# Optimization experiments

Measured on AMD Instinct MI355X. Metric: run time of the kernel, lower is better.

The kernel has to match this reference:

```python
import jax, jax.numpy as jnp
import numpy as np

N = 100000      # nodes
E = 3200000     # edges (avg degree 32)
NFEAT = 512
NHID = 256
NCLASS = 40
NLAYERS = 8
T1 = 5
T2 = 5
G1 = 1
G2 = 1
BETA = 0.5      # weight_beta
LAMDA = 0.5
ALPHA = 0.1
EPS = 1e-5


def ortho_trans(weight, T, groups):
    """Newton-Schulz orthogonalization (Ortho_Trans.forward)."""
    g = groups
    Z = weight.reshape(g, weight.shape[0] // g, -1)          # [g, d, k]
    Zc = Z - Z.mean(axis=-1, keepdims=True)
    S = jnp.einsum('gik,gjk->gij', Zc, Zc)                   # covariance [g, d, d]
    eye = jnp.eye(S.shape[-1], dtype=S.dtype)
    S = S + EPS * eye
    norm_S = jnp.sqrt(jnp.sum(S * S, axis=(1, 2), keepdims=True))  # fro norm
    S = S / norm_S
    B0 = jnp.broadcast_to(eye, S.shape)

    def body(B, _):
        B3 = B @ B @ B                                       # matrix_power3
        return 1.5 * B - 0.5 * (B3 @ S), None                # baddbmm(1.5,B,-0.5,B3,S)

    Bt, _ = jax.lax.scan(body, B0, None, length=T)
    W = (Bt @ Zc) / jnp.sqrt(norm_S)
    return W.reshape(weight.shape)


def setup_inputs() -> dict:
    key = jax.random.key(0)
    ks = jax.random.split(key, 8)
    stdv = 1.0 / np.sqrt(NHID)
    return {
        'x': jax.random.normal(ks[0], (N, NFEAT), dtype=jnp.float32),
        'edge_src': jax.random.randint(ks[1], (E,), 0, N, dtype=jnp.int32),
        'edge_dst': jax.random.randint(ks[2], (E,), 0, N, dtype=jnp.int32),
        'edge_weight': jax.random.uniform(ks[3], (E,), dtype=jnp.float32),
        'W0': jax.random.normal(ks[4], (NHID, NFEAT), dtype=jnp.float32) * 0.05,
        'b0': jnp.zeros((NHID,), dtype=jnp.float32),
        'convW': jax.random.uniform(ks[5], (NLAYERS, NHID, NHID), dtype=jnp.float32,
                                    minval=-stdv, maxval=stdv),
        'W1': jax.random.normal(ks[6], (NCLASS, NHID), dtype=jnp.float32) * 0.05,
        'b1': jnp.zeros((NCLASS,), dtype=jnp.float32),
    }


def reference(x, edge_src, edge_dst, edge_weight, W0, b0, convW, W1, b1):
    # fcs[0].weight is orthogonalized at init (Ortho=True)
    W0o = ortho_trans(W0, T1, G1)
    h = jax.nn.relu(x @ W0o.T + b0)                          # [N, NHID]
    h0 = h
    I = jnp.eye(NHID, dtype=h.dtype)
    ls = jnp.arange(1, NLAYERS + 1, dtype=h.dtype)

    def layer(h, inp):
        W, l = inp
        theta = jnp.log(LAMDA / l + 1.0)
        # sparse spmm: hi = adj @ h
        msgs = edge_weight[:, None] * h[edge_src]            # [E, NHID]
        hi = jax.ops.segment_sum(msgs, edge_dst, num_segments=N)
        support = (1.0 - ALPHA) * hi + ALPHA * h0            # variant=False -> r == support
        we = BETA * W + (1.0 - BETA) * I
        t = ortho_trans(we, T2, G2)
        out = jax.nn.relu(theta * (support @ t) + (1.0 - theta) * support)
        return out, None

    h, _ = jax.lax.scan(layer, h, (convW, ls))
    logits = h @ W1.T + b1
    return jax.nn.log_softmax(logits, axis=1)
```

## Files before the change

### kernel.cpp

```cpp
#include <hip/hip_runtime.h>
#include <math.h>

#define NNODES 100000
#define NEDGE  3200000
#define NF     512
#define NH     256
#define NC     40
#define NLAY   8
#define EPSV   1e-5f

typedef __attribute__((ext_vector_type(8))) short short8;
typedef __attribute__((ext_vector_type(4))) float floatx4;



__device__ __forceinline__ float block_sum_256(float v) {
    __shared__ float sb[8];
    #pragma unroll
    for (int off = 32; off; off >>= 1) v += __shfl_down(v, off, 64);
    if ((threadIdx.x & 63) == 0) sb[threadIdx.x >> 6] = v;
    __syncthreads();
    return sb[0] + sb[1] + sb[2] + sb[3];
}

__device__ __forceinline__ unsigned short bf16_rte(float a) {
    unsigned int u = __float_as_uint(a);
    return (unsigned short)((u + 0x7fffu + ((u >> 16) & 1u)) >> 16);
}
__device__ __forceinline__ unsigned int pack_bf2(float a, float b) {
    unsigned int ua = __float_as_uint(a), ub = __float_as_uint(b);
    ua = (ua + 0x7fffu + ((ua >> 16) & 1u)) >> 16;
    ub = (ub + 0x7fffu + ((ub >> 16) & 1u)) & 0xffff0000u;
    return ua | ub;
}


__global__ void k_hist(const int* __restrict__ dst, int* __restrict__ counts, int n) {
    int i = blockIdx.x * 256 + threadIdx.x;
    if (i < n) atomicAdd(&counts[dst[i]], 1);
}

__global__ void k_scan1(const int* __restrict__ in, int* __restrict__ out,
                        int* __restrict__ bsum, int n) {
    __shared__ int s[1024];
    int t = threadIdx.x, g = blockIdx.x * 1024 + t;
    int v = (g < n) ? in[g] : 0;
    s[t] = v; __syncthreads();
    for (int off = 1; off < 1024; off <<= 1) {
        int u = (t >= off) ? s[t - off] : 0;
        __syncthreads();
        s[t] += u;
        __syncthreads();
    }
    if (g < n) out[g] = s[t] - v;
    if (t == 1023) bsum[blockIdx.x] = s[1023];
}

__global__ void k_scan2(int* __restrict__ bsum, int nb) {
    __shared__ int s[128];
    int t = threadIdx.x;
    int v = (t < nb) ? bsum[t] : 0;
    s[t] = v; __syncthreads();
    for (int off = 1; off < 128; off <<= 1) {
        int u = (t >= off) ? s[t - off] : 0;
        __syncthreads();
        s[t] += u;
        __syncthreads();
    }
    if (t < nb) bsum[t] = s[t] - v;
}

__global__ void k_scan3(int* __restrict__ out, const int* __restrict__ bsum, int n) {
    int g = blockIdx.x * 1024 + threadIdx.x;
    if (g < n) out[g] += bsum[blockIdx.x];
}

__global__ void k_scatter(const int* __restrict__ src, const int* __restrict__ dst,
                          const float* __restrict__ w, const int* __restrict__ rstart,
                          int* __restrict__ cursor, unsigned int* __restrict__ epack, int n) {
    int i = blockIdx.x * 256 + threadIdx.x;
    if (i < n) {
        int d = dst[i];
        int pos = rstart[d] + atomicAdd(&cursor[d], 1);
        unsigned int wb = bf16_rte(w[i]) & 0x7FFFu;
        epack[pos] = ((unsigned int)src[i] << 15) | wb;
    }
}


__global__ void k_xbf16(const float* __restrict__ X, unsigned short* __restrict__ Xb, long n8) {
    long i = (long)blockIdx.x * 256 + threadIdx.x;
    if (i >= n8) return;
    const float* p = X + i * 8;
    float4 a = *(const float4*)p;
    float4 b = *(const float4*)(p + 4);
    uint4 o;
    o.x = pack_bf2(a.x, a.y); o.y = pack_bf2(a.z, a.w);
    o.z = pack_bf2(b.x, b.y); o.w = pack_bf2(b.z, b.w);
    *(uint4*)(Xb + i * 8) = o;
}


__global__ void k_zc0(const float* __restrict__ W0, float* __restrict__ Zc0) {
    int r = blockIdx.x, t = threadIdx.x;
    float a = W0[r * NF + t];
    float b = W0[r * NF + 256 + t];
    float mean = block_sum_256(a + b) * (1.0f / 512.0f);
    Zc0[r * NF + t]       = a - mean;
    Zc0[r * NF + 256 + t] = b - mean;
}

__global__ void k_zcC(const float* __restrict__ convW, float* __restrict__ ZcC) {
    int g = blockIdx.x >> 8, r = blockIdx.x & 255, t = threadIdx.x;
    float v = 0.5f * convW[((size_t)g * NH + r) * NH + t] + ((r == t) ? 0.5f : 0.0f);
    float mean = block_sum_256(v) * (1.0f / 256.0f);
    ZcC[((size_t)g * NH + r) * NH + t] = v - mean;
}

__global__ __launch_bounds__(256) void k_gram(const float* __restrict__ Zc0,
                                              const float* __restrict__ ZcC,
                                              float* __restrict__ S) {
    const int b = blockIdx.z;
    const float* A = (b == 0) ? Zc0 : (ZcC + (size_t)(b - 1) * 65536);
    const int K = (b == 0) ? 512 : 256;
    const int r0 = blockIdx.y * 64, c0 = blockIdx.x * 64;
    __shared__ float As[32][76], Bs[32][76];
    const int t = threadIdx.x, tx = t & 15, ty = t >> 4;
    const int lr = t >> 2, lk = (t & 3) * 4;
    float acc[4][4] = {};
    for (int k0 = 0; k0 < K; k0 += 32) {
        float4 a0 = *(const float4*)(A + (size_t)(r0 + lr) * K + k0 + lk);
        float4 a1 = *(const float4*)(A + (size_t)(r0 + lr) * K + k0 + lk + 16);
        As[lk + 0][lr] = a0.x; As[lk + 1][lr] = a0.y; As[lk + 2][lr] = a0.z; As[lk + 3][lr] = a0.w;
        As[lk + 16][lr] = a1.x; As[lk + 17][lr] = a1.y; As[lk + 18][lr] = a1.z; As[lk + 19][lr] = a1.w;
        float4 b0 = *(const float4*)(A + (size_t)(c0 + lr) * K + k0 + lk);
        float4 b1 = *(const float4*)(A + (size_t)(c0 + lr) * K + k0 + lk + 16);
        Bs[lk + 0][lr] = b0.x; Bs[lk + 1][lr] = b0.y; Bs[lk + 2][lr] = b0.z; Bs[lk + 3][lr] = b0.w;
        Bs[lk + 16][lr] = b1.x; Bs[lk + 17][lr] = b1.y; Bs[lk + 18][lr] = b1.z; Bs[lk + 19][lr] = b1.w;
        __syncthreads();
        #pragma unroll
        for (int kk = 0; kk < 32; kk++) {
            float a[4], bb[4];
            *(float4*)&a[0]  = *(const float4*)&As[kk][ty * 4];
            *(float4*)&bb[0] = *(const float4*)&Bs[kk][tx * 4];
            #pragma unroll
            for (int i = 0; i < 4; i++)
                #pragma unroll
                for (int j = 0; j < 4; j++) acc[i][j] = fmaf(a[i], bb[j], acc[i][j]);
        }
        __syncthreads();
    }
    #pragma unroll
    for (int i = 0; i < 4; i++)
        #pragma unroll
        for (int j = 0; j < 4; j++) {
            int r = r0 + ty * 4 + i, c = c0 + tx * 4 + j;
            float v = acc[i][j];
            if (r == c) v += EPSV;
            S[(size_t)b * 65536 + r * NH + c] = v;
        }
}

__global__ void k_fro(const float* __restrict__ S, float* __restrict__ scales) {
    __shared__ float sb[8];
    const int b = blockIdx.x, t = threadIdx.x;
    const float* p = S + (size_t)b * 65536;
    float s = 0.f;
    for (int i = t; i < 65536; i += 256) { float v = p[i]; s = fmaf(v, v, s); }
    #pragma unroll
    for (int off = 32; off; off >>= 1) s += __shfl_down(s, off, 64);
    if ((t & 63) == 0) sb[t >> 6] = s;
    __syncthreads();
    if (t == 0) {
        float nrm = sqrtf(sb[0] + sb[1] + sb[2] + sb[3]);
        scales[b]      = 1.0f / nrm;
        scales[16 + b] = rsqrtf(nrm);
    }
}

__global__ void k_initB1(const float* __restrict__ S, const float* __restrict__ scales,
                         float* __restrict__ B) {
    int i = blockIdx.x * 256 + threadIdx.x;
    int b = i >> 16, m = i & 65535;
    float v = -0.5f * scales[b] * S[i];
    if ((m >> 8) == (m & 255)) v += 1.5f;
    B[i] = v;
}

__global__ __launch_bounds__(256) void k_ns_pair(const float* __restrict__ Bb,
                                                 const float* __restrict__ Smat,
                                                 float* __restrict__ T1b,
                                                 float* __restrict__ T2b) {
    const int b = blockIdx.z;
    const int bb = (b < 9) ? b : b - 9;
    const float* A  = Bb + (size_t)bb * 65536;
    const float* Bm = (b < 9) ? A : (Smat + (size_t)bb * 65536);
    float* C = (b < 9) ? (T1b + (size_t)bb * 65536) : (T2b + (size_t)bb * 65536);
    const int r0 = blockIdx.y * 64, c0 = blockIdx.x * 64;
    __shared__ float As[32][76], Bs[32][76];
    const int t = threadIdx.x, tx = t & 15, ty = t >> 4;
    const int lr = t >> 2, lk = (t & 3) * 4;
    const int bk = t >> 3, bc = (t & 7) * 8;
    float acc[4][4] = {};
    for (int k0 = 0; k0 < 256; k0 += 32) {
        float4 a0 = *(const float4*)(A + (size_t)(r0 + lr) * 256 + k0 + lk);
        float4 a1 = *(const float4*)(A + (size_t)(r0 + lr) * 256 + k0 + lk + 16);
        As[lk + 0][lr] = a0.x; As[lk + 1][lr] = a0.y; As[lk + 2][lr] = a0.z; As[lk + 3][lr] = a0.w;
        As[lk + 16][lr] = a1.x; As[lk + 17][lr] = a1.y; As[lk + 18][lr] = a1.z; As[lk + 19][lr] = a1.w;
        float4 b0 = *(const float4*)(Bm + (size_t)(k0 + bk) * 256 + c0 + bc);
        float4 b1 = *(const float4*)(Bm + (size_t)(k0 + bk) * 256 + c0 + bc + 4);
        *(float4*)&Bs[bk][bc]     = b0;
        *(float4*)&Bs[bk][bc + 4] = b1;
        __syncthreads();
        #pragma unroll
        for (int kk = 0; kk < 32; kk++) {
            float a[4], bb2[4];
            *(float4*)&a[0]   = *(const float4*)&As[kk][ty * 4];
            *(float4*)&bb2[0] = *(const float4*)&Bs[kk][tx * 4];
            #pragma unroll
            for (int i = 0; i < 4; i++)
                #pragma unroll
                for (int j = 0; j < 4; j++) acc[i][j] = fmaf(a[i], bb2[j], acc[i][j]);
        }
        __syncthreads();
    }
    #pragma unroll
    for (int i = 0; i < 4; i++)
        #pragma unroll
        for (int j = 0; j < 4; j++)
            C[(size_t)(r0 + ty * 4 + i) * 256 + c0 + tx * 4 + j] = acc[i][j];
}

__global__ __launch_bounds__(256) void k_small_nn(const float* __restrict__ A0,
                                                  const float* __restrict__ B0,
                                                  float* __restrict__ C0,
                                                  int sA, int sB, int sC,
                                                  int K, int Ncols, int mode,
                                                  const float* __restrict__ scale) {
    const int b = blockIdx.z;
    const float* A = A0 + (size_t)b * sA;
    const float* Bm = B0 + (size_t)b * sB;
    float* C = C0 + (size_t)b * sC;
    const int r0 = blockIdx.y * 64, c0 = blockIdx.x * 64;
    __shared__ float As[32][76], Bs[32][76];
    const int t = threadIdx.x, tx = t & 15, ty = t >> 4;
    const int lr = t >> 2, lk = (t & 3) * 4;
    const int bk = t >> 3, bc = (t & 7) * 8;
    float acc[4][4] = {};
    for (int k0 = 0; k0 < K; k0 += 32) {
        float4 a0 = *(const float4*)(A + (size_t)(r0 + lr) * K + k0 + lk);
        float4 a1 = *(const float4*)(A + (size_t)(r0 + lr) * K + k0 + lk + 16);
        As[lk + 0][lr] = a0.x; As[lk + 1][lr] = a0.y; As[lk + 2][lr] = a0.z; As[lk + 3][lr] = a0.w;
        As[lk + 16][lr] = a1.x; As[lk + 17][lr] = a1.y; As[lk + 18][lr] = a1.z; As[lk + 19][lr] = a1.w;
        float4 b0 = *(const float4*)(Bm + (size_t)(k0 + bk) * Ncols + c0 + bc);
        float4 b1 = *(const float4*)(Bm + (size_t)(k0 + bk) * Ncols + c0 + bc + 4);
        *(float4*)&Bs[bk][bc]     = b0;
        *(float4*)&Bs[bk][bc + 4] = b1;
        __syncthreads();
        #pragma unroll
        for (int kk = 0; kk < 32; kk++) {
            float a[4], bb[4];
            *(float4*)&a[0]  = *(const float4*)&As[kk][ty * 4];
            *(float4*)&bb[0] = *(const float4*)&Bs[kk][tx * 4];
            #pragma unroll
            for (int i = 0; i < 4; i++)
                #pragma unroll
                for (int j = 0; j < 4; j++) acc[i][j] = fmaf(a[i], bb[j], acc[i][j]);
        }
        __syncthreads();
    }
    #pragma unroll
    for (int i = 0; i < 4; i++)
        #pragma unroll
        for (int j = 0; j < 4; j++) {
            size_t idx = (size_t)(r0 + ty * 4 + i) * Ncols + c0 + tx * 4 + j;
            if (mode == 1) C[idx] = 1.5f * C[idx] - 0.5f * scale[b] * acc[i][j];
            else C[idx] = scale[b] * acc[i][j];
        }
}


__global__ void k_prepM(const float* __restrict__ tbuf, unsigned short* __restrict__ Mpack) {
    int idx = blockIdx.x * 256 + threadIdx.x;
    int lane = idx & 63;
    int tg   = (idx >> 6) & 15;
    int s    = (idx >> 10) & 1;
    int c    = (idx >> 11) & 3;
    int l    = idx >> 13;
    float theta = logf(0.5f / (float)(l + 1) + 1.0f);
    float mtheta = 1.0f - theta;
    int n  = tg * 16 + (lane & 15);
    int k0 = c * 64 + s * 32 + (lane >> 4) * 8;
    const float* T = tbuf + (size_t)l * 65536;
    unsigned short o[8];
    #pragma unroll
    for (int j = 0; j < 8; j++) {
        int kp = k0 + j;
        int kn = (kp & 0xC0) | ((kp & 3) << 4) | ((kp >> 2) & 15);
        float v = theta * T[(size_t)kn * 256 + n] + ((kn == n) ? mtheta : 0.0f);
        o[j] = bf16_rte(v);
    }
    *(uint4*)(Mpack + (size_t)idx * 8) = *(uint4*)o;
}

__global__ void k_prepW0(const float* __restrict__ W0o, unsigned short* __restrict__ Wpack) {
    int idx = blockIdx.x * 256 + threadIdx.x;
    int lane = idx & 63;
    int tg   = (idx >> 6) & 15;
    int s    = (idx >> 10) & 1;
    int c    = idx >> 11;
    int n  = tg * 16 + (lane & 15);
    int k0 = c * 64 + s * 32 + (lane >> 4) * 8;
    const float* p = W0o + (size_t)n * NF + k0;
    unsigned short o[8];
    #pragma unroll
    for (int j = 0; j < 8; j++) o[j] = bf16_rte(p[j]);
    *(uint4*)(Wpack + (size_t)idx * 8) = *(uint4*)o;
}


__global__ __launch_bounds__(256) void k_fc0_mfma(const unsigned short* __restrict__ Xb,
                                                  const unsigned short* __restrict__ Wp,
                                                  const float* __restrict__ bias,
                                                  unsigned char* __restrict__ h0u8,
                                                  float* __restrict__ h0scale) {
    __shared__ int rmax[64];
    const int t = threadIdx.x, lane = t & 63, w = t >> 6;
    const int q = lane >> 4, m = lane & 15;
    const int r0 = blockIdx.x * 64;
    if (t < 64) rmax[t] = 0;
    floatx4 acc[4][4] = {};
    #pragma unroll
    for (int c = 0; c < 8; c++) {
        #pragma unroll
        for (int s = 0; s < 2; s++) {
            short8 afr[4];
            #pragma unroll
            for (int i = 0; i < 4; i++) {
                int row = r0 + i * 16 + m; if (row > NNODES - 1) row = NNODES - 1;
                afr[i] = *(const short8*)(Xb + (size_t)row * NF + c * 64 + s * 32 + q * 8);
            }
            #pragma unroll
            for (int tg = 0; tg < 4; tg++) {
                short8 bfr = *(const short8*)(Wp + (size_t)c * 16384 + s * 8192
                                              + (w * 4 + tg) * 512 + lane * 8);
                #pragma unroll
                for (int i = 0; i < 4; i++)
                    acc[i][tg] = __builtin_amdgcn_mfma_f32_16x16x32_bf16(afr[i], bfr, acc[i][tg], 0, 0, 0);
            }
        }
    }
    #pragma unroll
    for (int tg = 0; tg < 4; tg++) {
        float bv = bias[w * 64 + tg * 16 + m];
        #pragma unroll
        for (int i = 0; i < 4; i++)
            #pragma unroll
            for (int r = 0; r < 4; r++)
                acc[i][tg][r] = fmaxf(acc[i][tg][r] + bv, 0.f);
    }
    __syncthreads();
    #pragma unroll
    for (int i = 0; i < 4; i++)
        #pragma unroll
        for (int r = 0; r < 4; r++) {
            float mx = fmaxf(fmaxf(acc[i][0][r], acc[i][1][r]),
                             fmaxf(acc[i][2][r], acc[i][3][r]));
            mx = fmaxf(mx, __shfl_xor(mx, 1));
            mx = fmaxf(mx, __shfl_xor(mx, 2));
            mx = fmaxf(mx, __shfl_xor(mx, 4));
            mx = fmaxf(mx, __shfl_xor(mx, 8));
            if (m == 0) atomicMax(&rmax[i * 16 + q * 4 + r], __float_as_int(mx));
        }
    __syncthreads();
    #pragma unroll
    for (int i = 0; i < 4; i++)
        #pragma unroll
        for (int r = 0; r < 4; r++) {
            int row = r0 + i * 16 + q * 4 + r;
            if (row >= NNODES) continue;
            float rm = __int_as_float(rmax[i * 16 + q * 4 + r]);
            float qs = rm > 0.f ? 255.0f / rm : 0.f;
            unsigned int b0 = (unsigned int)fmaf(acc[i][0][r], qs, 0.5f);
            unsigned int b1 = (unsigned int)fmaf(acc[i][1][r], qs, 0.5f);
            unsigned int b2 = (unsigned int)fmaf(acc[i][2][r], qs, 0.5f);
            unsigned int b3 = (unsigned int)fmaf(acc[i][3][r], qs, 0.5f);
            *(unsigned int*)(h0u8 + (size_t)row * NH + w * 64 + m * 4) =
                b0 | (b1 << 8) | (b2 << 16) | (b3 << 24);
        }
    if (t < 64 && r0 + t < NNODES)
        h0scale[r0 + t] = __int_as_float(rmax[t]) * (1.0f / 255.0f);
}


__global__ __launch_bounds__(256) void k_spmm(const int* __restrict__ rstart,
                                              const int* __restrict__ counts,
                                              const unsigned int* __restrict__ epack,
                                              const unsigned char* __restrict__ hu8,
                                              const float* __restrict__ hscale,
                                              const unsigned char* __restrict__ h0u8,
                                              const float* __restrict__ h0scale,
                                              unsigned short* __restrict__ supbf) {
    __shared__ int2 se[4][64];
    const int wv = threadIdx.x >> 6, lane = threadIdx.x & 63;
    const int node = blockIdx.x * 4 + wv;
    const int start = rstart[node], deg = counts[node];
    float a0 = 0.f, a1 = 0.f, a2 = 0.f, a3 = 0.f;
    for (int base = 0; base < deg; base += 64) {
        int j = base + lane;
        if (j < deg) {
            unsigned int u = epack[start + j];
            int s = (int)(u >> 15);
            float wt = __uint_as_float((u & 0x7FFFu) << 16);
            se[wv][lane] = make_int2(s, __float_as_int(wt * hscale[s] * 0.9f));
        }
        int mm = deg - base; if (mm > 64) mm = 64;
        int e = 0;
        for (; e + 8 <= mm; e += 8) {
            float ww[8]; unsigned int g[8];
            #pragma unroll
            for (int u = 0; u < 8; u++) {
                int2 ed = se[wv][e + u];
                ww[u] = __int_as_float(ed.y);
                g[u] = *(const unsigned int*)(hu8 + ((size_t)ed.x << 8) + (lane << 2));
            }
            #pragma unroll
            for (int u = 0; u < 8; u++) {
                a0 = fmaf(ww[u], (float)(g[u] & 0xFFu), a0);
                a1 = fmaf(ww[u], (float)((g[u] >> 8) & 0xFFu), a1);
                a2 = fmaf(ww[u], (float)((g[u] >> 16) & 0xFFu), a2);
                a3 = fmaf(ww[u], (float)(g[u] >> 24), a3);
            }
        }
        for (; e < mm; e++) {
            int2 ed = se[wv][e];
            float ww = __int_as_float(ed.y);
            unsigned int g = *(const unsigned int*)(hu8 + ((size_t)ed.x << 8) + (lane << 2));
            a0 = fmaf(ww, (float)(g & 0xFFu), a0);
            a1 = fmaf(ww, (float)((g >> 8) & 0xFFu), a1);
            a2 = fmaf(ww, (float)((g >> 16) & 0xFFu), a2);
            a3 = fmaf(ww, (float)(g >> 24), a3);
        }
    }
    unsigned int rg = *(const unsigned int*)(h0u8 + ((size_t)node << 8) + (lane << 2));
    float rs = h0scale[node] * 0.1f;
    float o0 = fmaf(rs, (float)(rg & 0xFFu), a0);
    float o1 = fmaf(rs, (float)((rg >> 8) & 0xFFu), a1);
    float o2 = fmaf(rs, (float)((rg >> 16) & 0xFFu), a2);
    float o3 = fmaf(rs, (float)(rg >> 24), a3);
    uint2 ov;
    ov.x = pack_bf2(o0, o1);
    ov.y = pack_bf2(o2, o3);
    *(uint2*)(supbf + ((size_t)node << 8) + (lane << 2)) = ov;
}


__global__ __launch_bounds__(256) void k_gemm_layer(const unsigned short* __restrict__ Sbf,
                                                    const unsigned short* __restrict__ Mp,
                                                    unsigned char* __restrict__ out_u8,
                                                    float* __restrict__ out_scale,
                                                    unsigned short* __restrict__ out_bf) {
    __shared__ int rmax[64];
    const int t = threadIdx.x, lane = t & 63, w = t >> 6;
    const int q = lane >> 4, m = lane & 15;
    const int r0 = blockIdx.x * 64;
    if (t < 64) rmax[t] = 0;
    floatx4 acc[4][4] = {};
    #pragma unroll
    for (int c = 0; c < 4; c++) {
        #pragma unroll
        for (int s = 0; s < 2; s++) {
            short8 afr[4];
            #pragma unroll
            for (int i = 0; i < 4; i++) {
                int row = r0 + i * 16 + m; if (row > NNODES - 1) row = NNODES - 1;
                afr[i] = *(const short8*)(Sbf + (size_t)row * NH + c * 64 + s * 32 + q * 8);
            }
            #pragma unroll
            for (int tg = 0; tg < 4; tg++) {
                short8 bfr = *(const short8*)(Mp + (size_t)c * 16384 + s * 8192
                                              + (w * 4 + tg) * 512 + lane * 8);
                #pragma unroll
                for (int i = 0; i < 4; i++)
                    acc[i][tg] = __builtin_amdgcn_mfma_f32_16x16x32_bf16(afr[i], bfr, acc[i][tg], 0, 0, 0);
            }
        }
    }
    #pragma unroll
    for (int i = 0; i < 4; i++)
        #pragma unroll
        for (int tg = 0; tg < 4; tg++)
            #pragma unroll
            for (int r = 0; r < 4; r++)
                acc[i][tg][r] = fmaxf(acc[i][tg][r], 0.f);

    if (out_bf) {
        #pragma unroll
        for (int i = 0; i < 4; i++)
            #pragma unroll
            for (int tg = 0; tg < 4; tg++) {
                int col = w * 64 + tg * 16 + m;
                #pragma unroll
                for (int r = 0; r < 4; r++) {
                    int row = r0 + i * 16 + q * 4 + r;
                    if (row >= NNODES) continue;
                    out_bf[(size_t)row * NH + col] = bf16_rte(acc[i][tg][r]);
                }
            }
        return;
    }
    __syncthreads();
    #pragma unroll
    for (int i = 0; i < 4; i++)
        #pragma unroll
        for (int r = 0; r < 4; r++) {
            float mx = fmaxf(fmaxf(acc[i][0][r], acc[i][1][r]),
                             fmaxf(acc[i][2][r], acc[i][3][r]));
            mx = fmaxf(mx, __shfl_xor(mx, 1));
            mx = fmaxf(mx, __shfl_xor(mx, 2));
            mx = fmaxf(mx, __shfl_xor(mx, 4));
            mx = fmaxf(mx, __shfl_xor(mx, 8));
            if (m == 0) atomicMax(&rmax[i * 16 + q * 4 + r], __float_as_int(mx));
        }
    __syncthreads();
    #pragma unroll
    for (int i = 0; i < 4; i++)
        #pragma unroll
        for (int r = 0; r < 4; r++) {
            int row = r0 + i * 16 + q * 4 + r;
            if (row >= NNODES) continue;
            float rm = __int_as_float(rmax[i * 16 + q * 4 + r]);
            float qs = rm > 0.f ? 255.0f / rm : 0.f;
            unsigned int b0 = (unsigned int)fmaf(acc[i][0][r], qs, 0.5f);
            unsigned int b1 = (unsigned int)fmaf(acc[i][1][r], qs, 0.5f);
            unsigned int b2 = (unsigned int)fmaf(acc[i][2][r], qs, 0.5f);
            unsigned int b3 = (unsigned int)fmaf(acc[i][3][r], qs, 0.5f);
            *(unsigned int*)(out_u8 + (size_t)row * NH + w * 64 + m * 4) =
                b0 | (b1 << 8) | (b2 << 16) | (b3 << 24);
        }
    if (t < 64 && r0 + t < NNODES)
        out_scale[r0 + t] = __int_as_float(rmax[t]) * (1.0f / 255.0f);
}


__global__ __launch_bounds__(256) void k_logits(const unsigned short* __restrict__ hb,
                                                const float* __restrict__ W1,
                                                const float* __restrict__ b1,
                                                float* __restrict__ out, int nrows) {
    __shared__ float hs[32][260];
    __shared__ float Ws[40][260];
    __shared__ float ls[32][44];
    __shared__ float lse[32];
    const int t = threadIdx.x;
    const int row0 = blockIdx.x * 32;
    for (int i = t; i < 40 * 64; i += 256) {
        int c = i >> 6, k4 = i & 63;
        *(float4*)&Ws[c][k4 * 4] = *(const float4*)(W1 + (size_t)c * NH + k4 * 4);
    }
    for (int i = t; i < 32 * 32; i += 256) {
        int r = i >> 5, k8 = i & 31;
        int gr = row0 + r;
        uint4 v = make_uint4(0u, 0u, 0u, 0u);
        if (gr < nrows) v = *(const uint4*)(hb + ((size_t)gr << 8) + k8 * 8);
        float* d = &hs[r][k8 * 8];
        d[0] = __uint_as_float(v.x << 16); d[1] = __uint_as_float(v.x & 0xffff0000u);
        d[2] = __uint_as_float(v.y << 16); d[3] = __uint_as_float(v.y & 0xffff0000u);
        d[4] = __uint_as_float(v.z << 16); d[5] = __uint_as_float(v.z & 0xffff0000u);
        d[6] = __uint_as_float(v.w << 16); d[7] = __uint_as_float(v.w & 0xffff0000u);
    }
    __syncthreads();
    const int r = t & 31, cg = t >> 5;
    float acc[5];
    #pragma unroll
    for (int j = 0; j < 5; j++) acc[j] = b1[cg * 5 + j];
    for (int k = 0; k < NH; k++) {
        float hv = hs[r][k];
        #pragma unroll
        for (int j = 0; j < 5; j++) acc[j] = fmaf(hv, Ws[cg * 5 + j][k], acc[j]);
    }
    #pragma unroll
    for (int j = 0; j < 5; j++) ls[r][cg * 5 + j] = acc[j];
    __syncthreads();
    if (t < 32) {
        float m = -3.4e38f;
        for (int c = 0; c < NC; c++) m = fmaxf(m, ls[t][c]);
        float s = 0.f;
        for (int c = 0; c < NC; c++) s += expf(ls[t][c] - m);
        lse[t] = m + logf(s);
    }
    __syncthreads();
    for (int i = t; i < 32 * NC; i += 256) {
        int r2 = i / NC, c = i % NC;
        int gr = row0 + r2;
        if (gr < nrows) out[(size_t)gr * NC + c] = ls[r2][c] - lse[r2];
    }
}


extern "C" void kernel_launch(void* const* d_in, const int* in_sizes, int n_in,
                              void* d_out, int out_size, void* d_ws, size_t ws_size,
                              hipStream_t stream) {
    const float* x      = (const float*)d_in[0];
    const int*   e_src  = (const int*)d_in[1];
    const int*   e_dst  = (const int*)d_in[2];
    const float* e_w    = (const float*)d_in[3];
    const float* W0     = (const float*)d_in[4];
    const float* b0     = (const float*)d_in[5];
    const float* convW  = (const float*)d_in[6];
    const float* W1     = (const float*)d_in[7];
    const float* b1     = (const float*)d_in[8];
    float* out = (float*)d_out;

    char* ws = (char*)d_ws;
    const size_t OFF_H0U8   = 0;
    const size_t OFF_HU8A   = OFF_H0U8 + (size_t)NNODES * NH;
    const size_t OFF_HU8B   = OFF_HU8A + (size_t)NNODES * NH;
    const size_t OFF_H0SC   = OFF_HU8B + (size_t)NNODES * NH;
    const size_t OFF_SCA    = OFF_H0SC + (size_t)NNODES * 4;
    const size_t OFF_SCB    = OFF_SCA + (size_t)NNODES * 4;
    const size_t OFF_SUPBF  = OFF_SCB + (size_t)NNODES * 4;
    const size_t OFF_HBF    = OFF_SUPBF + (size_t)NNODES * NH * 2;
    const size_t OFF_XBF    = OFF_HBF + (size_t)NNODES * NH * 2;
    const size_t OFF_EPACK  = OFF_XBF + (size_t)NNODES * NF * 2;
    const size_t OFF_RSTART = OFF_EPACK + (size_t)NEDGE * 4;
    const size_t OFF_COUNTS = OFF_RSTART + (size_t)NNODES * 4;
    const size_t OFF_CURSOR = OFF_COUNTS + (size_t)NNODES * 4;
    const size_t OFF_BSUM   = OFF_CURSOR + (size_t)NNODES * 4;
    const size_t OFF_ZC0    = OFF_BSUM + 1024;
    const size_t OFF_ZCC    = OFF_ZC0 + 256 * 512 * 4;
    const size_t OFF_S      = OFF_ZCC + 8 * 65536 * 4;
    const size_t OFF_B      = OFF_S + 9 * 65536 * 4;
    const size_t OFF_T1     = OFF_B + 9 * 65536 * 4;
    const size_t OFF_T2     = OFF_T1 + 9 * 65536 * 4;
    const size_t OFF_T      = OFF_T2 + 9 * 65536 * 4;
    const size_t OFF_W0O    = OFF_T + 8 * 65536 * 4;
    const size_t OFF_SCALES = OFF_W0O + 256 * 512 * 4;
    const size_t OFF_MPACK  = OFF_SCALES + 1024;
    const size_t OFF_WPACK  = OFF_MPACK + 8 * 65536 * 2;

    unsigned char* h0u8 = (unsigned char*)(ws + OFF_H0U8);
    unsigned char* hu8A = (unsigned char*)(ws + OFF_HU8A);
    unsigned char* hu8B = (unsigned char*)(ws + OFF_HU8B);
    float* h0sc = (float*)(ws + OFF_H0SC);
    float* scA  = (float*)(ws + OFF_SCA);
    float* scB  = (float*)(ws + OFF_SCB);
    unsigned short* supbf = (unsigned short*)(ws + OFF_SUPBF);
    unsigned short* hbf   = (unsigned short*)(ws + OFF_HBF);
    unsigned short* xbf   = (unsigned short*)(ws + OFF_XBF);
    unsigned int* epack  = (unsigned int*)(ws + OFF_EPACK);
    int*    rstart = (int*)(ws + OFF_RSTART);
    int*    counts = (int*)(ws + OFF_COUNTS);
    int*    cursor = (int*)(ws + OFF_CURSOR);
    int*    bsum   = (int*)(ws + OFF_BSUM);
    float*  Zc0    = (float*)(ws + OFF_ZC0);
    float*  ZcC    = (float*)(ws + OFF_ZCC);
    float*  Smat   = (float*)(ws + OFF_S);
    float*  Bb     = (float*)(ws + OFF_B);
    float*  T1b    = (float*)(ws + OFF_T1);
    float*  T2b    = (float*)(ws + OFF_T2);
    float*  tbuf   = (float*)(ws + OFF_T);
    float*  W0o    = (float*)(ws + OFF_W0O);
    float*  scales = (float*)(ws + OFF_SCALES);
    unsigned short* Mpack = (unsigned short*)(ws + OFF_MPACK);
    unsigned short* Wpack = (unsigned short*)(ws + OFF_WPACK);

    (void)in_sizes; (void)n_in; (void)out_size; (void)ws_size;

    hipMemsetAsync(counts, 0, (size_t)NNODES * 4, stream);
    hipMemsetAsync(cursor, 0, (size_t)NNODES * 4, stream);
    k_hist<<<(NEDGE + 255) / 256, 256, 0, stream>>>(e_dst, counts, NEDGE);
    const int NB = (NNODES + 1023) / 1024;
    k_scan1<<<NB, 1024, 0, stream>>>(counts, rstart, bsum, NNODES);
    k_scan2<<<1, 128, 0, stream>>>(bsum, NB);
    k_scan3<<<NB, 1024, 0, stream>>>(rstart, bsum, NNODES);
    k_scatter<<<(NEDGE + 255) / 256, 256, 0, stream>>>(e_src, e_dst, e_w, rstart, cursor,
                                                       epack, NEDGE);

    const long N8 = (long)NNODES * NF / 8;
    k_xbf16<<<(int)((N8 + 255) / 256), 256, 0, stream>>>(x, xbf, N8);

    k_zc0<<<256, 256, 0, stream>>>(W0, Zc0);
    k_zcC<<<8 * 256, 256, 0, stream>>>(convW, ZcC);
    k_gram<<<dim3(4, 4, 9), 256, 0, stream>>>(Zc0, ZcC, Smat);
    k_fro<<<9, 256, 0, stream>>>(Smat, scales);
    k_initB1<<<9 * 256, 256, 0, stream>>>(Smat, scales, Bb);
    for (int it = 1; it < 5; it++) {
        k_ns_pair<<<dim3(4, 4, 18), 256, 0, stream>>>(Bb, Smat, T1b, T2b);
        k_small_nn<<<dim3(4, 4, 9), 256, 0, stream>>>(T1b, T2b, Bb, 65536, 65536, 65536,
                                                      256, 256, 1, scales);
    }
    k_small_nn<<<dim3(8, 4, 1), 256, 0, stream>>>(Bb, Zc0, W0o, 0, 0, 0,
                                                  256, 512, 2, scales + 16);
    k_small_nn<<<dim3(4, 4, 8), 256, 0, stream>>>(Bb + 65536, ZcC, tbuf, 65536, 65536, 65536,
                                                  256, 256, 2, scales + 17);

    k_prepM<<<256, 256, 0, stream>>>(tbuf, Mpack);
    k_prepW0<<<64, 256, 0, stream>>>(W0o, Wpack);

    const int GB = (NNODES + 63) / 64;
    k_fc0_mfma<<<GB, 256, 0, stream>>>(xbf, Wpack, b0, h0u8, h0sc);

    const unsigned char* hin = h0u8;
    const float* hinsc = h0sc;
    unsigned char* u8bufs[2] = { hu8A, hu8B };
    float* scbufs[2] = { scA, scB };
    for (int l = 1; l <= NLAY; l++) {
        k_spmm<<<NNODES / 4, 256, 0, stream>>>(rstart, counts, epack, hin, hinsc,
                                               h0u8, h0sc, supbf);
        const unsigned short* Mp = Mpack + (size_t)(l - 1) * 65536;
        if (l == NLAY) {
            k_gemm_layer<<<GB, 256, 0, stream>>>(supbf, Mp, nullptr, nullptr, hbf);
        } else {
            unsigned char* ou = u8bufs[(l - 1) & 1];
            float* os = scbufs[(l - 1) & 1];
            k_gemm_layer<<<GB, 256, 0, stream>>>(supbf, Mp, ou, os, nullptr);
            hin = ou; hinsc = os;
        }
    }

    k_logits<<<(NNODES + 31) / 32, 256, 0, stream>>>(hbf, W1, b1, out, NNODES);
}
```

Measured before the change: 2.435 ms.

## Replace atomic edge scatter with two-pass bucketed binning for CSR build

The per-edge scatter, which did a global atomic and a random write for every edge, is replaced by two passes. In the first pass, edges are binned into 128-node buckets using shared-memory histograms and one global atomic per bucket per block, and written to a staging buffer. In the second pass, one block per bucket sorts its edges into destination order in LDS and writes them out contiguously. The aim is to cut global atomics and scattered writes. The cost is an extra pass through staging memory and a fixed per-bucket LDS capacity (BCAP) that would overflow if degrees were highly skewed.

```diff
diff --git a/kernel.cpp b/kernel.cpp
--- a/kernel.cpp
+++ b/kernel.cpp
@@ -8,6 +8,10 @@
 #define NC     40
 #define NLAY   8
 #define EPSV   1e-5f
+
+#define NBUK 782
+#define EPB  16384
+#define BCAP 6144
 
 typedef __attribute__((ext_vector_type(8))) short short8;
 typedef __attribute__((ext_vector_type(4))) float floatx4;
@@ -75,16 +79,91 @@
     if (g < n) out[g] += bsum[blockIdx.x];
 }
 
-__global__ void k_scatter(const int* __restrict__ src, const int* __restrict__ dst,
-                          const float* __restrict__ w, const int* __restrict__ rstart,
-                          int* __restrict__ cursor, unsigned int* __restrict__ epack, int n) {
-    int i = blockIdx.x * 256 + threadIdx.x;
-    if (i < n) {
-        int d = dst[i];
-        int pos = rstart[d] + atomicAdd(&cursor[d], 1);
-        unsigned int wb = bf16_rte(w[i]) & 0x7FFFu;
-        epack[pos] = ((unsigned int)src[i] << 15) | wb;
-    }
+__global__ void k_initcur(const int* __restrict__ rstart, int* __restrict__ gcur) {
+    int b = blockIdx.x * 256 + threadIdx.x;
+    if (b < NBUK) gcur[b] = rstart[b << 7];
+}
+
+__global__ __launch_bounds__(1024) void k_binA(const int* __restrict__ src,
+                                               const int* __restrict__ dst,
+                                               const float* __restrict__ w,
+                                               int* __restrict__ gcur,
+                                               uint2* __restrict__ gstage) {
+    __shared__ int lhist[1024];
+    __shared__ int lrun[NBUK];
+    __shared__ int lcnt[NBUK];
+    const int t = threadIdx.x;
+    lhist[t] = 0;
+    if (t < NBUK) lcnt[t] = 0;
+    __syncthreads();
+    const int e0 = blockIdx.x * EPB;
+    unsigned int pk[16]; int bk[16]; int dl[16];
+    #pragma unroll
+    for (int i = 0; i < 16; i++) {
+        int e = e0 + i * 1024 + t;
+        bk[i] = -1;
+        if (e < NEDGE) {
+            int d = dst[e];
+            bk[i] = d >> 7; dl[i] = d & 127;
+            unsigned int wb = bf16_rte(w[e]) & 0x7FFFu;
+            pk[i] = ((unsigned int)src[e] << 15) | wb;
+            atomicAdd(&lhist[bk[i]], 1);
+        }
+    }
+    __syncthreads();
+    if (t < NBUK) {
+        int c = lhist[t];
+        if (c > 0) lrun[t] = atomicAdd(&gcur[t], c);
+    }
+    __syncthreads();
+    #pragma unroll
+    for (int i = 0; i < 16; i++) {
+        if (bk[i] >= 0) {
+            int p = lrun[bk[i]] + atomicAdd(&lcnt[bk[i]], 1);
+            gstage[p] = make_uint2(pk[i], (unsigned int)dl[i]);
+        }
+    }
+}
+
+__global__ __launch_bounds__(256) void k_binB(const int* __restrict__ rstart,
+                                              const uint2* __restrict__ gstage,
+                                              unsigned int* __restrict__ epack) {
+    __shared__ unsigned int  spk[BCAP];
+    __shared__ unsigned char sdl[BCAP];
+    __shared__ unsigned int  lout[BCAP];
+    __shared__ int lh[256];
+    const int b = blockIdx.x, t = threadIdx.x;
+    const int base = rstart[b << 7];
+    const int nn = (b + 1) << 7;
+    const int end = (nn < NNODES) ? rstart[nn] : NEDGE;
+    const int cnt = end - base;
+    lh[t] = 0;
+    __syncthreads();
+    for (int i = t; i < cnt; i += 256) {
+        uint2 e = gstage[base + i];
+        spk[i] = e.x;
+        int d = (int)(e.y & 127u);
+        sdl[i] = (unsigned char)d;
+        atomicAdd(&lh[d], 1);
+    }
+    __syncthreads();
+    int v = lh[t];
+    for (int off = 1; off < 256; off <<= 1) {
+        int u = (t >= off) ? lh[t - off] : 0;
+        __syncthreads();
+        lh[t] += u;
+        __syncthreads();
+    }
+    int excl = lh[t] - v;
+    __syncthreads();
+    lh[t] = excl;
+    __syncthreads();
+    for (int i = t; i < cnt; i += 256) {
+        int p = atomicAdd(&lh[sdl[i]], 1);
+        lout[p] = spk[i];
+    }
+    __syncthreads();
+    for (int i = t; i < cnt; i += 256) epack[base + i] = lout[i];
 }
 
 
@@ -650,7 +729,7 @@
     unsigned int* epack  = (unsigned int*)(ws + OFF_EPACK);
     int*    rstart = (int*)(ws + OFF_RSTART);
     int*    counts = (int*)(ws + OFF_COUNTS);
-    int*    cursor = (int*)(ws + OFF_CURSOR);
+    int*    gcur   = (int*)(ws + OFF_CURSOR);
     int*    bsum   = (int*)(ws + OFF_BSUM);
     float*  Zc0    = (float*)(ws + OFF_ZC0);
     float*  ZcC    = (float*)(ws + OFF_ZCC);
@@ -663,18 +742,19 @@
     float*  scales = (float*)(ws + OFF_SCALES);
     unsigned short* Mpack = (unsigned short*)(ws + OFF_MPACK);
     unsigned short* Wpack = (unsigned short*)(ws + OFF_WPACK);
+    uint2* gstage = (uint2*)(ws + OFF_SUPBF);
 
     (void)in_sizes; (void)n_in; (void)out_size; (void)ws_size;
 
     hipMemsetAsync(counts, 0, (size_t)NNODES * 4, stream);
-    hipMemsetAsync(cursor, 0, (size_t)NNODES * 4, stream);
     k_hist<<<(NEDGE + 255) / 256, 256, 0, stream>>>(e_dst, counts, NEDGE);
     const int NB = (NNODES + 1023) / 1024;
     k_scan1<<<NB, 1024, 0, stream>>>(counts, rstart, bsum, NNODES);
     k_scan2<<<1, 128, 0, stream>>>(bsum, NB);
     k_scan3<<<NB, 1024, 0, stream>>>(rstart, bsum, NNODES);
-    k_scatter<<<(NEDGE + 255) / 256, 256, 0, stream>>>(e_src, e_dst, e_w, rstart, cursor,
-                                                       epack, NEDGE);
+    k_initcur<<<4, 256, 0, stream>>>(rstart, gcur);
+    k_binA<<<(NEDGE + EPB - 1) / EPB, 1024, 0, stream>>>(e_src, e_dst, e_w, gcur, gstage);
+    k_binB<<<NBUK, 256, 0, stream>>>(rstart, gstage, epack);
 
     const long N8 = (long)NNODES * NF / 8;
     k_xbf16<<<(int)((N8 + 255) / 256), 256, 0, stream>>>(x, xbf, N8);
```

Result: faster. 2.321 ms (-4.7%).
